# Kernel tuning notes

Hardware: AMD Instinct MI355X
Metric: run time of the kernel (lower is better)

The kernel has to match this reference:

```python
import jax, jax.numpy as jnp
import numpy as np
import math

V, T, D, H, L, B = 50257, 1024, 768, 12, 6, 2
FF = 4 * D
HD = D // H

def layernorm(x, g, b, eps=1e-5):
    mu = jnp.mean(x, axis=-1, keepdims=True)
    var = jnp.var(x, axis=-1, keepdims=True)
    return (x - mu) * jax.lax.rsqrt(var + eps) * g + b

def new_gelu(x):
    # Faithful to the (buggy) NewGelu: tanh arg = sqrt(2/pi) * 0.044715 * x**4
    c = math.sqrt(2.0 / math.pi)
    return 0.5 * x * (1.0 + jnp.tanh(c * (x * 0.044715 * jnp.power(x, 3))))

def setup_inputs() -> dict:
    key = jax.random.key(0)
    ks = jax.random.split(key, 18)
    n = lambda k, shape, s=0.02: (jax.random.normal(k, shape, dtype=jnp.float32) * s)
    return {
        "ids": jax.random.randint(ks[0], (B, T), 0, V),
        "wte": n(ks[1], (V, D)),
        "wpe": n(ks[2], (T, D)),
        "W_qkv": n(ks[3], (L, D, 3 * D)),
        "b_qkv": jnp.zeros((L, 3 * D), jnp.float32),
        "W_o": n(ks[4], (L, D, D)),
        "b_o": jnp.zeros((L, D), jnp.float32),
        "ln1_g": jnp.ones((L, D), jnp.float32),
        "ln1_b": jnp.zeros((L, D), jnp.float32),
        "W1": n(ks[5], (L, D, FF)),
        "b1": jnp.zeros((L, FF), jnp.float32),
        "W2": n(ks[6], (L, FF, D)),
        "b2": jnp.zeros((L, D), jnp.float32),
        "lnf_g": jnp.ones((D,), jnp.float32),
        "lnf_b": jnp.zeros((D,), jnp.float32),
        "W_head": n(ks[7], (D, V)),
        "b_head": jnp.zeros((V,), jnp.float32),
    }

def reference(ids, wte, wpe, W_qkv, b_qkv, W_o, b_o, ln1_g, ln1_b,
              W1, b1, W2, b2, lnf_g, lnf_b, W_head, b_head):
    t = ids.shape[1]
    x = wte[ids] + wpe[:t][None]  # [B,T,D]
    scale = 1.0 / math.sqrt(HD)
    for l in range(L):
        qkv = x @ W_qkv[l] + b_qkv[l]                 # [B,T,3D]
        q, k, v = jnp.split(qkv, 3, axis=-1)
        q = q.reshape(-1, t, H, HD).transpose(0, 2, 1, 3)  # [B,H,T,hd]
        k = k.reshape(-1, t, H, HD).transpose(0, 2, 1, 3)
        v = v.reshape(-1, t, H, HD).transpose(0, 2, 1, 3)
        # NOTE: mask buffer is all-ones in the source, so NO causal masking.
        att = jax.nn.softmax(jnp.einsum('bhqd,bhkd->bhqk', q, k) * scale, axis=-1)
        y = jnp.einsum('bhqk,bhkd->bhqd', att, v)
        y = y.transpose(0, 2, 1, 3).reshape(-1, t, D)
        y = y @ W_o[l] + b_o[l]
        x = layernorm(y, ln1_g[l], ln1_b[l]) + x      # ln1 AFTER attn, per source
        h = new_gelu(x @ W1[l] + b1[l]) @ W2[l] + b2[l]  # ln2 unused, per source
        x = h + x
    x = layernorm(x, lnf_g, lnf_b)
    logits = x @ W_head + b_head
    return logits
```

## Files before the change

kernel.cpp:

```cpp
#include <hip/hip_runtime.h>
#include <hip/hip_bf16.h>
#include <math.h>
#include <stdint.h>

#define NL 6
#define NB 2
#define ST 1024
#define ND 768
#define NH 12
#define HD 64
#define NFF 3072
#define NV 50257
#define ND3 2304
#define NM (NB * ST)

typedef short bf16x4 __attribute__((ext_vector_type(4)));
typedef short bf16x8 __attribute__((ext_vector_type(8)));
typedef float f32x4  __attribute__((ext_vector_type(4)));

typedef __attribute__((address_space(3))) void as3_void;
typedef __attribute__((address_space(1))) void as1_void;

__device__ __forceinline__ void async_copy16(const void* g, void* lds) {
  __builtin_amdgcn_global_load_lds((const as1_void*)(uintptr_t)g,
                                   (as3_void*)(uint32_t)(uintptr_t)lds,
                                   16, 0, 0);
}

__device__ __forceinline__ unsigned short f2bf(float f) {
  union { float f; uint32_t u; } v; v.f = f;
  return (unsigned short)((v.u + 0x7fffu + ((v.u >> 16) & 1u)) >> 16);
}

__device__ __forceinline__ bf16x8 frag16(const unsigned short* p) {
  return *(const bf16x8*)p;
}

template <int N>
__device__ __forceinline__ void wait_vm_barrier() {
  if constexpr (N == 8)      asm volatile("s_waitcnt vmcnt(8)\n\ts_barrier" ::: "memory");
  else if constexpr (N == 6) asm volatile("s_waitcnt vmcnt(6)\n\ts_barrier" ::: "memory");
  else if constexpr (N == 4) asm volatile("s_waitcnt vmcnt(4)\n\ts_barrier" ::: "memory");
  else                       asm volatile("s_waitcnt vmcnt(0)\n\ts_barrier" ::: "memory");
}
__device__ __forceinline__ void lgkm_barrier() {
  asm volatile("s_waitcnt lgkmcnt(0)\n\ts_barrier" ::: "memory");
}

#define MFMA(a, b, c) __builtin_amdgcn_mfma_f32_16x16x32_bf16((a), (b), (c), 0, 0, 0)

__device__ __forceinline__ float gelu_buggy(float x) {
  const float c = 0.7978845608028654f;
  float x2 = x * x;
  return 0.5f * x * (1.0f + tanhf(c * 0.044715f * x2 * x2));
}

enum { EP_QKV = 0, EP_PROJ, EP_FF1, EP_FF2, EP_HEAD };

template <int EPI, int TM, int TN, int WN, int NW, int BK, int NBUF>
__global__ __launch_bounds__(NW * 64)
void gemm_bt(const unsigned short* __restrict__ A,
             const unsigned short* __restrict__ BT,
             const float* __restrict__ bias,
             float* __restrict__ Cf,
             unsigned short* __restrict__ Cb,
             const float* __restrict__ resid,
             unsigned short* __restrict__ vT,
             int M, int N, int K)
{
  constexpr int WM = NW / WN;
  constexpr int FM = TM / WM / 16;
  constexpr int FN = TN / WN / 16;
  constexpr int SL = BK / 8;
  constexpr int RS = (BK == 32) ? 1 : 0;
  constexpr int RPC = 1024 / (BK * 2);
  constexpr int CA = TM / RPC / NW;
  constexpr int CB = TN / RPC / NW;
  constexpr int LPT = CA + CB;
  constexpr int KK = BK / 32;
  constexpr int DEPTH = NBUF - 1;
  __shared__ __align__(16) unsigned short As[NBUF][TM * BK];
  __shared__ __align__(16) unsigned short Bs[NBUF][TN * BK];
  const int tid = threadIdx.x;
  const int w = tid >> 6, l = tid & 63;
  const int g = l >> 4, r = l & 15;
  const int wm = (w / WN) * (FM * 16);
  const int wn = (w % WN) * (FN * 16);

  const int nbx = gridDim.x;
  const int nwg = nbx * gridDim.y;
  int bid = blockIdx.y * nbx + blockIdx.x;
  if ((nwg & 7) == 0) bid = (bid & 7) * (nwg >> 3) + (bid >> 3);
  const int m0 = (bid % nbx) * TM, n0 = (bid / nbx) * TN;

  const int sr = l / (BK / 8);
  const int se = ((l & (SL - 1)) ^ ((sr >> RS) & (SL - 1))) * 8;
  long aoff[CA];
  long boff[CB];
#pragma unroll
  for (int c = 0; c < CA; ++c) {
    const int arow = (w * CA + c) * RPC + sr;
    aoff[c] = (long)(m0 + arow) * K + se;
  }
#pragma unroll
  for (int c = 0; c < CB; ++c) {
    int brow = n0 + (w * CB + c) * RPC + sr;
    if (brow > N - 1) brow = N - 1;
    boff[c] = (long)brow * K + se;
  }

  f32x4 acc[FM][FN] = {};

  auto stage = [&](int t, int buf) {
    const long k0 = (long)t * BK;
#pragma unroll
    for (int c = 0; c < CA; ++c)
      async_copy16(A + aoff[c] + k0, &As[buf][(w * CA + c) * 512]);
#pragma unroll
    for (int c = 0; c < CB; ++c)
      async_copy16(BT + boff[c] + k0, &Bs[buf][(w * CB + c) * 512]);
  };

  auto compute = [&](int buf) {
#pragma unroll
    for (int kk = 0; kk < KK; ++kk) {
      bf16x8 af[FM], bf[FN];
#pragma unroll
      for (int mi = 0; mi < FM; ++mi)
        af[mi] = frag16(&As[buf][(wm + mi * 16 + r) * BK +
                                 (((kk * 4 + g) ^ ((r >> RS) & (SL - 1))) * 8)]);
#pragma unroll
      for (int ni = 0; ni < FN; ++ni)
        bf[ni] = frag16(&Bs[buf][(wn + ni * 16 + r) * BK +
                                 (((kk * 4 + g) ^ ((r >> RS) & (SL - 1))) * 8)]);
      __builtin_amdgcn_s_setprio(1);
#pragma unroll
      for (int mi = 0; mi < FM; ++mi)
#pragma unroll
        for (int ni = 0; ni < FN; ++ni)
          acc[mi][ni] = MFMA(af[mi], bf[ni], acc[mi][ni]);
      __builtin_amdgcn_s_setprio(0);
    }
  };

  const int nt = K / BK;
  stage(0, 0);
  if (DEPTH == 2) stage(1, 1);
  int cur = 0, nxt = DEPTH;
  for (int t = 0; t < nt; ++t) {
    const bool have_next = (t + DEPTH) < nt;
    if (have_next) stage(t + DEPTH, nxt);
    if (have_next && DEPTH == 2)       wait_vm_barrier<2 * LPT>();
    else if (have_next || (DEPTH == 2 && t + 1 < nt)) wait_vm_barrier<LPT>();
    else                               wait_vm_barrier<0>();
    compute(cur);
    if (t + 1 < nt) lgkm_barrier();
    cur = (cur + 1 == NBUF) ? 0 : cur + 1;
    nxt = (nxt + 1 == NBUF) ? 0 : nxt + 1;
  }

#pragma unroll
  for (int mi = 0; mi < FM; ++mi) {
#pragma unroll
    for (int ni = 0; ni < FN; ++ni) {
      const int col = n0 + wn + ni * 16 + r;
      if (EPI == EP_HEAD && col >= N) continue;
      const float bb = bias[col];
      if (EPI == EP_QKV && col >= 2 * ND) {
        const int hv = (col - 2 * ND) >> 6, d = (col - 2 * ND) & 63;
        short4 vv;
#pragma unroll
        for (int q = 0; q < 4; ++q)
          vv[q] = (short)f2bf(acc[mi][ni][q] + bb);
        const int row = m0 + wm + mi * 16 + g * 4;
        const int bb_ = row >> 10, t4 = row & 1023;
        *(short4*)&vT[(((long)bb_ * NH + hv) * HD + d) * ST + t4] = vv;
        continue;
      }
#pragma unroll
      for (int q = 0; q < 4; ++q) {
        const int row = m0 + wm + mi * 16 + g * 4 + q;
        float v = acc[mi][ni][q] + bb;
        if constexpr (EPI == EP_QKV) {
          Cb[(long)row * N + col] = f2bf(v);
        } else if constexpr (EPI == EP_PROJ) {
          Cf[(long)row * N + col] = v;
        } else if constexpr (EPI == EP_FF1) {
          Cb[(long)row * N + col] = f2bf(gelu_buggy(v));
        } else if constexpr (EPI == EP_FF2) {
          float o = v + resid[(long)row * N + col];
          Cf[(long)row * N + col] = o;
          Cb[(long)row * N + col] = f2bf(o);
        } else {
          Cf[(long)row * N + col] = v;
        }
      }
    }
  }
}

__global__ __launch_bounds__(256)
void attn_kernel(const unsigned short* __restrict__ qkv,
                 const unsigned short* __restrict__ vT,
                 unsigned short* __restrict__ y)
{
  constexpr int LS = 72;
  __shared__ __align__(16) unsigned short Qs[64 * LS];
  __shared__ __align__(16) unsigned short Ks[64 * LS];
  __shared__ __align__(16) unsigned short Vt[64 * LS];
  __shared__ __align__(16) unsigned short Ps[64 * LS];
  const int tid = threadIdx.x;
  const int w = tid >> 6, l = tid & 63;
  const int g = l >> 4, r = l & 15;
  const int q0 = blockIdx.x * 64;
  const int b = blockIdx.y / NH, h = blockIdx.y % NH;
  const long rb = (long)b * ST;
  const long vbase = ((long)b * NH + h) * HD * ST;
  const int srow = tid >> 3, sc8 = (tid & 7) * 8;

#pragma unroll
  for (int p = 0; p < 2; ++p) {
    const int row = p * 32 + srow;
    bf16x8 v = *(const bf16x8*)&qkv[(rb + q0 + row) * ND3 + h * HD + sc8];
    *(bf16x8*)&Qs[row * LS + sc8] = v;
  }
  __syncthreads();
  bf16x8 aq[2];
#pragma unroll
  for (int kk = 0; kk < 2; ++kk)
    aq[kk] = *(const bf16x8*)&Qs[(w * 16 + r) * LS + kk * 32 + g * 8];

  float m_run[4] = {-1e30f, -1e30f, -1e30f, -1e30f};
  float l_run[4] = {0.f, 0.f, 0.f, 0.f};
  f32x4 acc_o[4] = {};

  for (int kt = 0; kt < ST / 64; ++kt) {
#pragma unroll
    for (int p = 0; p < 2; ++p) {
      const int row = p * 32 + srow;
      *(bf16x8*)&Ks[row * LS + sc8] =
          *(const bf16x8*)&qkv[(rb + kt * 64 + row) * ND3 + ND + h * HD + sc8];
      *(bf16x8*)&Vt[row * LS + sc8] =
          *(const bf16x8*)&vT[vbase + (long)row * ST + kt * 64 + sc8];
    }
    __syncthreads();

    f32x4 s_acc[4] = {};
#pragma unroll
    for (int kk = 0; kk < 2; ++kk) {
#pragma unroll
      for (int ni = 0; ni < 4; ++ni) {
        bf16x8 bk = *(const bf16x8*)&Ks[(ni * 16 + r) * LS + kk * 32 + g * 8];
        s_acc[ni] = MFMA(aq[kk], bk, s_acc[ni]);
      }
    }

    float mloc[4];
#pragma unroll
    for (int q = 0; q < 4; ++q) {
      float mx = fmaxf(fmaxf(s_acc[0][q], s_acc[1][q]), fmaxf(s_acc[2][q], s_acc[3][q]));
      mloc[q] = mx * 0.125f;
    }
#pragma unroll
    for (int mask = 1; mask < 16; mask <<= 1)
#pragma unroll
      for (int q = 0; q < 4; ++q)
        mloc[q] = fmaxf(mloc[q], __shfl_xor(mloc[q], mask, 64));

    float alpha[4], psum[4] = {0.f, 0.f, 0.f, 0.f};
#pragma unroll
    for (int q = 0; q < 4; ++q) {
      const float mn = fmaxf(m_run[q], mloc[q]);
      alpha[q] = __expf(m_run[q] - mn);
      m_run[q] = mn;
    }
#pragma unroll
    for (int ni = 0; ni < 4; ++ni)
#pragma unroll
      for (int q = 0; q < 4; ++q) {
        const float p = __expf(s_acc[ni][q] * 0.125f - m_run[q]);
        psum[q] += p;
        Ps[(w * 16 + g * 4 + q) * LS + ni * 16 + r] = f2bf(p);
      }
#pragma unroll
    for (int mask = 1; mask < 16; mask <<= 1)
#pragma unroll
      for (int q = 0; q < 4; ++q) psum[q] += __shfl_xor(psum[q], mask, 64);
#pragma unroll
    for (int q = 0; q < 4; ++q) l_run[q] = l_run[q] * alpha[q] + psum[q];
#pragma unroll
    for (int ni = 0; ni < 4; ++ni)
#pragma unroll
      for (int q = 0; q < 4; ++q) acc_o[ni][q] *= alpha[q];

    asm volatile("s_waitcnt lgkmcnt(0)" ::: "memory");
    __builtin_amdgcn_sched_barrier(0);

#pragma unroll
    for (int kk = 0; kk < 2; ++kk) {
      bf16x8 ap = *(const bf16x8*)&Ps[(w * 16 + r) * LS + kk * 32 + g * 8];
#pragma unroll
      for (int ni = 0; ni < 4; ++ni) {
        bf16x8 bv = *(const bf16x8*)&Vt[(ni * 16 + r) * LS + kk * 32 + g * 8];
        acc_o[ni] = MFMA(ap, bv, acc_o[ni]);
      }
    }
    __syncthreads();
  }

#pragma unroll
  for (int ni = 0; ni < 4; ++ni)
#pragma unroll
    for (int q = 0; q < 4; ++q) {
      const int row = q0 + w * 16 + g * 4 + q;
      const int col = h * HD + ni * 16 + r;
      y[(rb + row) * ND + col] = f2bf(acc_o[ni][q] / l_run[q]);
    }
}

template <bool RESID>
__global__ __launch_bounds__(256)
void ln_kernel(const float* __restrict__ in, const float* __restrict__ resid,
               const float* __restrict__ gamma, const float* __restrict__ beta,
               float* __restrict__ out_f, unsigned short* __restrict__ out_b)
{
  __shared__ float wred[8];
  const int row = blockIdx.x, tid = threadIdx.x;
  float v[3];
#pragma unroll
  for (int j = 0; j < 3; ++j) v[j] = in[(long)row * ND + tid + j * 256];
  float s = v[0] + v[1] + v[2];
#pragma unroll
  for (int m = 1; m < 64; m <<= 1) s += __shfl_xor(s, m, 64);
  if ((tid & 63) == 0) wred[tid >> 6] = s;
  __syncthreads();
  const float mean = (wred[0] + wred[1] + wred[2] + wred[3]) * (1.0f / ND);
  float d[3];
#pragma unroll
  for (int j = 0; j < 3; ++j) d[j] = v[j] - mean;
  float s2 = d[0] * d[0] + d[1] * d[1] + d[2] * d[2];
#pragma unroll
  for (int m = 1; m < 64; m <<= 1) s2 += __shfl_xor(s2, m, 64);
  if ((tid & 63) == 0) wred[4 + (tid >> 6)] = s2;
  __syncthreads();
  const float var = (wred[4] + wred[5] + wred[6] + wred[7]) * (1.0f / ND);
  const float rstd = rsqrtf(var + 1e-5f);
#pragma unroll
  for (int j = 0; j < 3; ++j) {
    const int c = tid + j * 256;
    float o = d[j] * rstd * gamma[c] + beta[c];
    if (RESID) o += resid[(long)row * ND + c];
    if (out_f) out_f[(long)row * ND + c] = o;
    if (out_b) out_b[(long)row * ND + c] = f2bf(o);
  }
}

__global__ __launch_bounds__(256)
void embed_kernel(const int* __restrict__ ids, const float* __restrict__ wte,
                  const float* __restrict__ wpe, float* __restrict__ x,
                  unsigned short* __restrict__ xb)
{
  const int t = blockIdx.x, tid = threadIdx.x;
  const int tok = ids[t];
  const int pos = t & (ST - 1);
#pragma unroll
  for (int j = 0; j < 3; ++j) {
    const int c = tid + j * 256;
    const float v = wte[(long)tok * ND + c] + wpe[(long)pos * ND + c];
    x[(long)t * ND + c] = v;
    xb[(long)t * ND + c] = f2bf(v);
  }
}

__global__ __launch_bounds__(256)
void transpose_bf16(const float* __restrict__ in, unsigned short* __restrict__ out,
                    int R, int C)
{
  __shared__ float tile[64][33];
  const long z = (long)blockIdx.z * R * C;
  const int c0 = blockIdx.x * 32, r0 = blockIdx.y * 64;
  const int tx = threadIdx.x & 31, ty = threadIdx.x >> 5;
#pragma unroll
  for (int j = 0; j < 8; ++j) {
    const int rr = r0 + j * 8 + ty, cc = c0 + tx;
    if (cc < C) tile[j * 8 + ty][tx] = in[z + (long)rr * C + cc];
  }
  __syncthreads();
  const int rx = threadIdx.x & 63, cy = threadIdx.x >> 6;
#pragma unroll
  for (int j = 0; j < 8; ++j) {
    const int cc = c0 + j * 4 + cy;
    if (cc < C) out[z + (long)cc * R + r0 + rx] = f2bf(tile[rx][j * 4 + cy]);
  }
}

extern "C" void kernel_launch(void* const* d_in, const int* in_sizes, int n_in,
                              void* d_out, int out_size, void* d_ws, size_t ws_size,
                              hipStream_t stream)
{
  const int*   ids    = (const int*)d_in[0];
  const float* wte    = (const float*)d_in[1];
  const float* wpe    = (const float*)d_in[2];
  const float* W_qkv  = (const float*)d_in[3];
  const float* b_qkv  = (const float*)d_in[4];
  const float* W_o    = (const float*)d_in[5];
  const float* b_o    = (const float*)d_in[6];
  const float* ln1_g  = (const float*)d_in[7];
  const float* ln1_b  = (const float*)d_in[8];
  const float* W1     = (const float*)d_in[9];
  const float* b1     = (const float*)d_in[10];
  const float* W2     = (const float*)d_in[11];
  const float* b2     = (const float*)d_in[12];
  const float* lnf_g  = (const float*)d_in[13];
  const float* lnf_b  = (const float*)d_in[14];
  const float* W_head = (const float*)d_in[15];
  const float* b_head = (const float*)d_in[16];
  float* out = (float*)d_out;
  (void)in_sizes; (void)n_in; (void)out_size; (void)ws_size;

  char* ws = (char*)d_ws;
  size_t off = 0;
  auto alloc = [&](size_t bytes) -> void* {
    void* p = (void*)(ws + off);
    off = (off + bytes + 255) & ~(size_t)255;
    return p;
  };
  unsigned short* wqkvT = (unsigned short*)alloc((size_t)NL * ND3 * ND * 2);
  unsigned short* woT   = (unsigned short*)alloc((size_t)NL * ND * ND * 2);
  unsigned short* w1T   = (unsigned short*)alloc((size_t)NL * NFF * ND * 2);
  unsigned short* w2T   = (unsigned short*)alloc((size_t)NL * ND * NFF * 2);
  unsigned short* whT   = (unsigned short*)alloc((size_t)NV * ND * 2);
  float*          xf    = (float*)alloc((size_t)NM * ND * 4);
  unsigned short* xb    = (unsigned short*)alloc((size_t)NM * ND * 2);
  unsigned short* qkvb  = (unsigned short*)alloc((size_t)NM * ND3 * 2);
  unsigned short* yb    = (unsigned short*)alloc((size_t)NM * ND * 2);
  float*          aof   = (float*)alloc((size_t)NM * ND * 4);
  unsigned short* h1b   = (unsigned short*)alloc((size_t)NM * NFF * 2);
  unsigned short* xlnb  = (unsigned short*)alloc((size_t)NM * ND * 2);
  unsigned short* vtb   = (unsigned short*)alloc((size_t)NB * NH * HD * ST * 2);

  dim3 tb(256);
  dim3 tb128(128);
  dim3 tb512(512);
  transpose_bf16<<<dim3(ND3 / 32, ND / 64, NL), tb, 0, stream>>>(W_qkv, wqkvT, ND, ND3);
  transpose_bf16<<<dim3(ND / 32, ND / 64, NL), tb, 0, stream>>>(W_o, woT, ND, ND);
  transpose_bf16<<<dim3(NFF / 32, ND / 64, NL), tb, 0, stream>>>(W1, w1T, ND, NFF);
  transpose_bf16<<<dim3(ND / 32, NFF / 64, NL), tb, 0, stream>>>(W2, w2T, NFF, ND);
  transpose_bf16<<<dim3((NV + 31) / 32, ND / 64, 1), tb, 0, stream>>>(W_head, whT, ND, NV);

  embed_kernel<<<dim3(NM), tb, 0, stream>>>(ids, wte, wpe, xf, xb);

  for (int l = 0; l < NL; ++l) {
    gemm_bt<EP_QKV, 128, 64, 2, 4, 64, 2><<<dim3(NM / 128, ND3 / 64), tb, 0, stream>>>(
        xb, wqkvT + (size_t)l * ND3 * ND, b_qkv + (size_t)l * ND3,
        nullptr, qkvb, nullptr, vtb, NM, ND3, ND);
    attn_kernel<<<dim3(ST / 64, NB * NH), tb, 0, stream>>>(qkvb, vtb, yb);
    gemm_bt<EP_PROJ, 64, 64, 2, 2, 64, 2><<<dim3(NM / 64, ND / 64), tb128, 0, stream>>>(
        yb, woT + (size_t)l * ND * ND, b_o + (size_t)l * ND,
        aof, nullptr, nullptr, nullptr, NM, ND, ND);
    ln_kernel<true><<<dim3(NM), tb, 0, stream>>>(
        aof, xf, ln1_g + (size_t)l * ND, ln1_b + (size_t)l * ND, xf, xb);
    gemm_bt<EP_FF1, 128, 64, 2, 4, 64, 2><<<dim3(NM / 128, NFF / 64), tb, 0, stream>>>(
        xb, w1T + (size_t)l * NFF * ND, b1 + (size_t)l * NFF,
        nullptr, h1b, nullptr, nullptr, NM, NFF, ND);
    gemm_bt<EP_FF2, 64, 64, 2, 2, 64, 2><<<dim3(NM / 64, ND / 64), tb128, 0, stream>>>(
        h1b, w2T + (size_t)l * ND * NFF, b2 + (size_t)l * ND,
        xf, xb, xf, nullptr, NM, ND, NFF);
  }
  ln_kernel<false><<<dim3(NM), tb, 0, stream>>>(xf, nullptr, lnf_g, lnf_b, nullptr, xlnb);
  gemm_bt<EP_HEAD, 256, 256, 4, 8, 32, 3><<<dim3(NM / 256, (NV + 255) / 256), tb512, 0, stream>>>(
      xlnb, whT, b_head, out, nullptr, nullptr, nullptr, NM, NV, ND);
}
```

Measured before the change: 1.132 ms.

## Add dedicated 8-phase pipelined head GEMM kernel with XCD-aware block remap

Replaces the generic gemm_bt call for the vocab projection with a specialised 256x256 kernel. It double-buffers LDS with BK=64 and interleaves async global-to-LDS loads across eight compute phases per K-tile pair. It raises MFMA priority with s_setprio, remaps block IDs across the eight XCDs for L2 locality, and clamps out-of-range B rows rather than branching. The aim is to hide load latency behind MFMA work on the largest GEMM. The cost is hand-tuned vmcnt accounting that breaks easily, plus heavy LDS use (128KB) that limits occupancy.

```diff
diff --git a/kernel.cpp b/kernel.cpp
--- a/kernel.cpp
+++ b/kernel.cpp
@@ -40,6 +40,7 @@
 __device__ __forceinline__ void wait_vm_barrier() {
   if constexpr (N == 8)      asm volatile("s_waitcnt vmcnt(8)\n\ts_barrier" ::: "memory");
   else if constexpr (N == 6) asm volatile("s_waitcnt vmcnt(6)\n\ts_barrier" ::: "memory");
+  else if constexpr (N == 5) asm volatile("s_waitcnt vmcnt(5)\n\ts_barrier" ::: "memory");
   else if constexpr (N == 4) asm volatile("s_waitcnt vmcnt(4)\n\ts_barrier" ::: "memory");
   else                       asm volatile("s_waitcnt vmcnt(0)\n\ts_barrier" ::: "memory");
 }
@@ -164,7 +165,6 @@
 #pragma unroll
     for (int ni = 0; ni < FN; ++ni) {
       const int col = n0 + wn + ni * 16 + r;
-      if (EPI == EP_HEAD && col >= N) continue;
       const float bb = bias[col];
       if (EPI == EP_QKV && col >= 2 * ND) {
         const int hv = (col - 2 * ND) >> 6, d = (col - 2 * ND) & 63;
@@ -191,9 +191,142 @@
           float o = v + resid[(long)row * N + col];
           Cf[(long)row * N + col] = o;
           Cb[(long)row * N + col] = f2bf(o);
-        } else {
-          Cf[(long)row * N + col] = v;
         }
+      }
+    }
+  }
+}
+
+__global__ __launch_bounds__(512, 2)
+void gemm_head_8ph(const unsigned short* __restrict__ A,
+                   const unsigned short* __restrict__ BT,
+                   const float* __restrict__ bias,
+                   float* __restrict__ Cf,
+                   int M, int N, int K)
+{
+  __shared__ __align__(16) unsigned short As[2][256 * 64];
+  __shared__ __align__(16) unsigned short Bs[2][256 * 64];
+  const int tid = threadIdx.x;
+  const int w = tid >> 6, l = tid & 63;
+  const int g = l >> 4, r = l & 15;
+  const int wm = (w >> 2) * 128;
+  const int wn = (w & 3) * 64;
+
+  const int nbx = gridDim.x;
+  const int nwg = nbx * gridDim.y;
+  int bid = blockIdx.y * nbx + blockIdx.x;
+  bid = (bid & 7) * (nwg >> 3) + (bid >> 3);
+  const int m0 = (bid % nbx) * 256, n0 = (bid / nbx) * 256;
+
+  const int sr = l >> 3;
+  const int se = ((l & 7) ^ sr) * 8;
+  const int a_base0 = (w < 4 ? 0 : 128) + (w & 3) * 8;
+
+  auto stageA = [&](int tt, int q) {
+    const int row = a_base0 + q * 32;
+    async_copy16(A + (long)(m0 + row + sr) * K + tt * 64 + se,
+                 &As[tt & 1][row * 64]);
+  };
+  auto stageB = [&](int tt, int h) {
+#pragma unroll
+    for (int c = 0; c < 2; ++c) {
+      const int row = h * 128 + w * 16 + c * 8;
+      int brow = n0 + row + sr; if (brow > N - 1) brow = N - 1;
+      async_copy16(BT + (long)brow * K + tt * 64 + se,
+                   &Bs[tt & 1][row * 64]);
+    }
+  };
+  auto ldA = [&](int buf, int mi, int kk) -> bf16x8 {
+    const int row = wm + mi * 16 + r;
+    return frag16(&As[buf][row * 64 + (((kk * 4 + g) ^ (r & 7)) * 8)]);
+  };
+  auto ldB = [&](int buf, int ni, int kk) -> bf16x8 {
+    const int row = wn + ni * 16 + r;
+    return frag16(&Bs[buf][row * 64 + (((kk * 4 + g) ^ (r & 7)) * 8)]);
+  };
+
+  f32x4 acc[8][4] = {};
+  bf16x8 bfr[4][2];
+
+#define DO_PHASE(buf, p, first)                                           \
+  do {                                                                    \
+    bf16x8 af[2][2];                                                      \
+    _Pragma("unroll")                                                     \
+    for (int i_ = 0; i_ < 2; ++i_)                                        \
+      _Pragma("unroll")                                                   \
+      for (int k_ = 0; k_ < 2; ++k_)                                      \
+        af[i_][k_] = ldA(buf, 2 * (p) + i_, k_);                          \
+    if (first) {                                                          \
+      _Pragma("unroll")                                                   \
+      for (int n_ = 0; n_ < 4; ++n_)                                      \
+        _Pragma("unroll")                                                 \
+        for (int k_ = 0; k_ < 2; ++k_)                                    \
+          bfr[n_][k_] = ldB(buf, n_, k_);                                 \
+    }                                                                     \
+    asm volatile("s_barrier" ::: "memory");                               \
+    asm volatile("s_waitcnt lgkmcnt(0)" ::: "memory");                    \
+    __builtin_amdgcn_sched_barrier(0);                                    \
+    __builtin_amdgcn_s_setprio(1);                                        \
+    _Pragma("unroll")                                                     \
+    for (int i_ = 0; i_ < 2; ++i_)                                        \
+      _Pragma("unroll")                                                   \
+      for (int n_ = 0; n_ < 4; ++n_)                                      \
+        _Pragma("unroll")                                                 \
+        for (int k_ = 0; k_ < 2; ++k_)                                    \
+          acc[2 * (p) + i_][n_] =                                         \
+              MFMA(af[i_][k_], bfr[n_][k_], acc[2 * (p) + i_][n_]);       \
+    __builtin_amdgcn_s_setprio(0);                                        \
+    asm volatile("s_barrier" ::: "memory");                               \
+  } while (0)
+
+  const int nt = K >> 6;
+  const int niter = nt >> 1;
+
+#pragma unroll
+  for (int q = 0; q < 4; ++q) stageA(0, q);
+  stageB(0, 0); stageB(0, 1);
+#pragma unroll
+  for (int q = 0; q < 4; ++q) stageA(1, q);
+  stageB(1, 0); stageB(1, 1);
+
+  for (int it = 0; it < niter; ++it) {
+    const int T = 2 * it;
+    if (it > 0) { stageA(T + 1, 3); stageB(T + 1, 0); }
+    if (it == 0) wait_vm_barrier<8>(); else wait_vm_barrier<5>();
+    DO_PHASE(0, 0, true);
+    if (T + 2 < nt) stageA(T + 2, 0);
+    if (it > 0) stageB(T + 1, 1);
+    DO_PHASE(0, 1, false);
+    if (T + 2 < nt) stageA(T + 2, 1);
+    DO_PHASE(0, 2, false);
+    if (T + 2 < nt) stageA(T + 2, 2);
+    DO_PHASE(0, 3, false);
+    if (T + 2 < nt) { stageA(T + 2, 3); stageB(T + 2, 0); }
+    if (it == 0) wait_vm_barrier<6>();
+    else if (it == niter - 1) wait_vm_barrier<0>();
+    else wait_vm_barrier<5>();
+    DO_PHASE(1, 0, true);
+    if (T + 3 < nt) stageA(T + 3, 0);
+    if (T + 2 < nt) stageB(T + 2, 1);
+    DO_PHASE(1, 1, false);
+    if (T + 3 < nt) stageA(T + 3, 1);
+    DO_PHASE(1, 2, false);
+    if (T + 3 < nt) stageA(T + 3, 2);
+    DO_PHASE(1, 3, false);
+  }
+#undef DO_PHASE
+
+#pragma unroll
+  for (int mi = 0; mi < 8; ++mi) {
+#pragma unroll
+    for (int ni = 0; ni < 4; ++ni) {
+      const int col = n0 + wn + ni * 16 + r;
+      if (col >= N) continue;
+      const float bb = bias[col];
+#pragma unroll
+      for (int q = 0; q < 4; ++q) {
+        const int row = m0 + wm + mi * 16 + g * 4 + q;
+        Cf[(long)row * N + col] = acc[mi][ni][q] + bb;
       }
     }
   }
@@ -468,6 +601,6 @@
         xf, xb, xf, nullptr, NM, ND, NFF);
   }
   ln_kernel<false><<<dim3(NM), tb, 0, stream>>>(xf, nullptr, lnf_g, lnf_b, nullptr, xlnb);
-  gemm_bt<EP_HEAD, 256, 256, 4, 8, 32, 3><<<dim3(NM / 256, (NV + 255) / 256), tb512, 0, stream>>>(
-      xlnb, whT, b_head, out, nullptr, nullptr, nullptr, NM, NV, ND);
-}
+  gemm_head_8ph<<<dim3(NM / 256, (NV + 255) / 256), tb512, 0, stream>>>(
+      xlnb, whT, b_head, out, NM, NV, ND);
+}
```

Measured after the change: 1.105 ms. -2.4%, faster.
